# Optimization experiments

Hardware: AMD Instinct MI355X
Metric: run time of the kernel (lower is better)

## Reference

```python
import jax, jax.numpy as jnp
import numpy as np

N = 100000
E = 1600000
IN_FEATS = 512
N_CLASSES = 40
H1, D1 = 8, 8
H2, D2 = 1, N_CLASSES


def gat_conv(x, src, dst, W, al, ar, b, H, D):
    # x: [N, F] -> h: [N, H, D]
    n = x.shape[0]
    h = (x @ W).reshape(n, H, D)
    el = (h * al[None]).sum(-1)  # [N, H]
    er = (h * ar[None]).sum(-1)  # [N, H]
    e = jax.nn.leaky_relu(el[src] + er[dst], 0.2)  # [E, H]
    # segment softmax over destination neighborhoods
    emax = jax.ops.segment_max(e, dst, num_segments=n)  # [N, H]
    ee = jnp.exp(e - emax[dst])
    denom = jax.ops.segment_sum(ee, dst, num_segments=n)  # [N, H]
    a = ee / (denom[dst] + 1e-9)  # [E, H]
    m = h[src] * a[:, :, None]  # [E, H, D]
    out = jax.ops.segment_sum(m, dst, num_segments=n)  # [N, H, D]
    return out + b.reshape(1, H, D)


def setup_inputs() -> dict:
    key = jax.random.key(0)
    ks = jax.random.split(key, 12)
    g1 = 1.0 / np.sqrt(IN_FEATS)
    g2 = 1.0 / np.sqrt(H1 * D1)
    return {
        "x": jax.random.normal(ks[0], (N, IN_FEATS), jnp.float32),
        "src": jax.random.randint(ks[1], (E,), 0, N, jnp.int32),
        "dst": jax.random.randint(ks[2], (E,), 0, N, jnp.int32),
        "W1": jax.random.normal(ks[3], (IN_FEATS, H1 * D1), jnp.float32) * g1,
        "al1": jax.random.normal(ks[4], (H1, D1), jnp.float32) * 0.1,
        "ar1": jax.random.normal(ks[5], (H1, D1), jnp.float32) * 0.1,
        "b1": jnp.zeros((H1 * D1,), jnp.float32),
        "W2": jax.random.normal(ks[6], (H1 * D1, H2 * D2), jnp.float32) * g2,
        "al2": jax.random.normal(ks[7], (H2, D2), jnp.float32) * 0.1,
        "ar2": jax.random.normal(ks[8], (H2, D2), jnp.float32) * 0.1,
        "b2": jnp.zeros((H2 * D2,), jnp.float32),
    }


def reference(x, src, dst, W1, al1, ar1, b1, W2, al2, ar2, b2):
    h = gat_conv(x, src, dst, W1, al1, ar1, b1, H1, D1)  # [N, 8, 8]
    h = jax.nn.elu(h.reshape(N, H1 * D1))  # [N, 64]
    h = gat_conv(h, src, dst, W2, al2, ar2, b2, H2, D2).mean(axis=1)  # [N, n_classes]
    return jax.nn.log_softmax(h, axis=1)
```

## Files before the change

### kernel.cpp

```cpp
#include <hip/hip_runtime.h>
#include <hip/hip_bf16.h>
#include <math.h>

#define NCLS 40
#define H2S 64
#define PWG 256
#define BSH 9
#define NBMAX 512
#define SRCB 23
#define CSRCAP 14336

typedef __attribute__((ext_vector_type(8))) short bf16x8;
typedef __attribute__((ext_vector_type(4))) float f32x4;

__device__ inline float bf2f(ushort u) {
    unsigned v = ((unsigned)u) << 16;
    float f;
    __builtin_memcpy(&f, &v, 4);
    return f;
}
__device__ inline ushort f2bf(float f) {
    unsigned v;
    __builtin_memcpy(&v, &f, 4);
    unsigned r = (v + 0x7FFFu + ((v >> 16) & 1u)) >> 16;
    return (ushort)r;
}

__global__ __launch_bounds__(256) void conv_prep_kernel(
    const float* __restrict__ W1, ushort* __restrict__ W1t,
    const float* __restrict__ W2, const float* __restrict__ al2,
    const float* __restrict__ ar2, float* __restrict__ wal2,
    float* __restrict__ war2)
{
    if (blockIdx.x < 128) {
        int id = blockIdx.x * 256 + threadIdx.x;
        int k = id >> 6, c = id & 63;
        W1t[c * 512 + k] = f2bf(W1[k * 64 + c]);
    } else {
        int k = threadIdx.x;
        if (k < 64) {
            float a = 0.f, b = 0.f;
            for (int c = 0; c < NCLS; c++) {
                float w = W2[k * NCLS + c];
                a += w * al2[c];
                b += w * ar2[c];
            }
            wal2[k] = a;
            war2[k] = b;
        }
    }
}

__global__ __launch_bounds__(256) void gemm1_mfma_kernel(
    const float* __restrict__ x, const ushort* __restrict__ W1t,
    const float* __restrict__ al1, const float* __restrict__ ar1,
    ushort* __restrict__ h1b, float* __restrict__ el1,
    float* __restrict__ er1, int Nn)
{
    __shared__ ushort As[64 * 72];
    __shared__ ushort Bs[64 * 72];
    const int t = threadIdx.x;
    const int lane = t & 63, w = t >> 6;
    const int tile = blockIdx.x * 64;

    f32x4 acc[4] = {};

    const int sr = t >> 2;
    const int sk = (t & 3) * 16;
    const int arow = tile + sr;
    const bool rowok = arow < Nn;
    const float* xrow = x + (size_t)arow * 512;
    const ushort* wrow = W1t + (size_t)sr * 512;

    const int r = lane & 15, g = lane >> 4;

    float4 f0 = make_float4(0.f, 0.f, 0.f, 0.f), f1 = f0, f2 = f0, f3 = f0;
    bf16x8 bv0, bv1;
    if (rowok) {
        f0 = *(const float4*)(xrow + sk);
        f1 = *(const float4*)(xrow + sk + 4);
        f2 = *(const float4*)(xrow + sk + 8);
        f3 = *(const float4*)(xrow + sk + 12);
    }
    bv0 = *(const bf16x8*)(wrow + sk);
    bv1 = *(const bf16x8*)(wrow + sk + 8);

    for (int k0 = 0; k0 < 512; k0 += 64) {
        bf16x8 av0, av1;
        av0[0] = (short)f2bf(f0.x); av0[1] = (short)f2bf(f0.y);
        av0[2] = (short)f2bf(f0.z); av0[3] = (short)f2bf(f0.w);
        av0[4] = (short)f2bf(f1.x); av0[5] = (short)f2bf(f1.y);
        av0[6] = (short)f2bf(f1.z); av0[7] = (short)f2bf(f1.w);
        av1[0] = (short)f2bf(f2.x); av1[1] = (short)f2bf(f2.y);
        av1[2] = (short)f2bf(f2.z); av1[3] = (short)f2bf(f2.w);
        av1[4] = (short)f2bf(f3.x); av1[5] = (short)f2bf(f3.y);
        av1[6] = (short)f2bf(f3.z); av1[7] = (short)f2bf(f3.w);
        *(bf16x8*)&As[sr * 72 + sk] = av0;
        *(bf16x8*)&As[sr * 72 + sk + 8] = av1;
        *(bf16x8*)&Bs[sr * 72 + sk] = bv0;
        *(bf16x8*)&Bs[sr * 72 + sk + 8] = bv1;
        __syncthreads();

        int k1 = k0 + 64;
        if (k1 < 512) {
            if (rowok) {
                f0 = *(const float4*)(xrow + k1 + sk);
                f1 = *(const float4*)(xrow + k1 + sk + 4);
                f2 = *(const float4*)(xrow + k1 + sk + 8);
                f3 = *(const float4*)(xrow + k1 + sk + 12);
            }
            bv0 = *(const bf16x8*)(wrow + k1 + sk);
            bv1 = *(const bf16x8*)(wrow + k1 + sk + 8);
        }

        bf16x8 af0 = *(const bf16x8*)&As[(w * 16 + r) * 72 + g * 8];
        bf16x8 af1 = *(const bf16x8*)&As[(w * 16 + r) * 72 + 32 + g * 8];
#pragma unroll
        for (int cb = 0; cb < 4; cb++) {
            bf16x8 bf0 = *(const bf16x8*)&Bs[(cb * 16 + r) * 72 + g * 8];
            acc[cb] = __builtin_amdgcn_mfma_f32_16x16x32_bf16(af0, bf0, acc[cb], 0, 0, 0);
        }
#pragma unroll
        for (int cb = 0; cb < 4; cb++) {
            bf16x8 bf1 = *(const bf16x8*)&Bs[(cb * 16 + r) * 72 + 32 + g * 8];
            acc[cb] = __builtin_amdgcn_mfma_f32_16x16x32_bf16(af1, bf1, acc[cb], 0, 0, 0);
        }
        __syncthreads();
    }

    float alv[4], arv[4];
#pragma unroll
    for (int cb = 0; cb < 4; cb++) {
        alv[cb] = al1[cb * 16 + r];
        arv[cb] = ar1[cb * 16 + r];
    }
#pragma unroll
    for (int v = 0; v < 4; v++) {
        int row = tile + w * 16 + g * 4 + v;
        bool ok = row < Nn;
#pragma unroll
        for (int cb = 0; cb < 4; cb++) {
            if (ok) h1b[(size_t)row * 64 + cb * 16 + r] = f2bf(acc[cb][v]);
            float pel = acc[cb][v] * alv[cb];
            float per = acc[cb][v] * arv[cb];
            pel += __shfl_xor(pel, 1); per += __shfl_xor(per, 1);
            pel += __shfl_xor(pel, 2); per += __shfl_xor(per, 2);
            pel += __shfl_xor(pel, 4); per += __shfl_xor(per, 4);
            if (ok && (r & 7) == 0) {
                int head = cb * 2 + (r >> 3);
                el1[row * 8 + head] = pel;
                er1[row * 8 + head] = per;
            }
        }
    }
}

__global__ __launch_bounds__(256) void hist_kernel(const int* __restrict__ dst,
                                                   int* __restrict__ hist,
                                                   int Ee, int chunk, int NB)
{
    __shared__ int lh[NBMAX];
    const int wg = blockIdx.x, tid = threadIdx.x;
    for (int i = tid; i < NB; i += 256) lh[i] = 0;
    __syncthreads();
    const int beg = wg * chunk;
    const int endv = min(Ee, beg + chunk);
    for (int i = beg + tid; i < endv; i += 256) atomicAdd(&lh[dst[i] >> BSH], 1);
    __syncthreads();
    for (int b = tid; b < NB; b += 256) hist[b * PWG + wg] = lh[b];
}

__global__ __launch_bounds__(256) void scanA_kernel(int* __restrict__ hist,
                                                    int* __restrict__ bucketTot)
{
    __shared__ int s[256];
    const int b = blockIdx.x, tid = threadIdx.x;
    int v = hist[b * PWG + tid];
    s[tid] = v;
    __syncthreads();
#pragma unroll
    for (int o = 1; o < 256; o <<= 1) {
        int t = (tid >= o) ? s[tid - o] : 0;
        __syncthreads();
        s[tid] += t;
        __syncthreads();
    }
    hist[b * PWG + tid] = s[tid] - v;
    if (tid == 255) bucketTot[b] = s[255];
}

__global__ __launch_bounds__(256) void scanB_kernel(const int* __restrict__ bucketTot,
                                                    int* __restrict__ bucketBase,
                                                    int NB, int Ee)
{
    __shared__ int s[256];
    const int tid = threadIdx.x;
    int v = (tid < NB) ? bucketTot[tid] : 0;
    s[tid] = v;
    __syncthreads();
#pragma unroll
    for (int o = 1; o < 256; o <<= 1) {
        int t = (tid >= o) ? s[tid - o] : 0;
        __syncthreads();
        s[tid] += t;
        __syncthreads();
    }
    if (tid < NB) bucketBase[tid] = s[tid] - v;
    if (tid == 0) bucketBase[NB] = Ee;
}

__global__ __launch_bounds__(256) void partition_kernel(const int* __restrict__ src,
                                                        const int* __restrict__ dst,
                                                        const int* __restrict__ hist,
                                                        const int* __restrict__ bucketBase,
                                                        unsigned* __restrict__ ebuf,
                                                        int Ee, int chunk, int NB)
{
    __shared__ int cur[NBMAX];
    const int wg = blockIdx.x, tid = threadIdx.x;
    for (int b = tid; b < NB; b += 256) cur[b] = hist[b * PWG + wg] + bucketBase[b];
    __syncthreads();
    const int beg = wg * chunk;
    const int endv = min(Ee, beg + chunk);
    for (int i = beg + tid; i < endv; i += 256) {
        int d = dst[i];
        int p = atomicAdd(&cur[d >> BSH], 1);
        ebuf[p] = ((unsigned)(d & ((1 << BSH) - 1)) << SRCB) | (unsigned)src[i];
    }
}

__global__ __launch_bounds__(512) void bucket_csr_kernel(const unsigned* __restrict__ ebuf,
                                                         const int* __restrict__ bucketBase,
                                                         int* __restrict__ row_start,
                                                         int* __restrict__ perm_src,
                                                         int Nn, int Ee, int NB)
{
    __shared__ unsigned stage[CSRCAP];
    __shared__ int cnt[512];
    __shared__ int s[512];
    __shared__ int cur[512];
    const int b = blockIdx.x, tid = threadIdx.x;
    const int base = b << BSH;
    const int bb = bucketBase[b], be = bucketBase[b + 1];
    const int m = be - bb;

    cnt[tid] = 0;
    __syncthreads();
    for (int idx = tid; idx < m; idx += 512) {
        unsigned pk = ebuf[bb + idx];
        if (idx < CSRCAP) stage[idx] = pk;
        atomicAdd(&cnt[pk >> SRCB], 1);
    }
    __syncthreads();
    int v = cnt[tid];
    s[tid] = v;
    __syncthreads();
#pragma unroll
    for (int o = 1; o < 512; o <<= 1) {
        int t = (tid >= o) ? s[tid - o] : 0;
        __syncthreads();
        s[tid] += t;
        __syncthreads();
    }
    const int off = bb + s[tid] - v;
    const int node = base + tid;
    if (node < Nn) row_start[node] = off;
    cur[tid] = off;
    __syncthreads();
    for (int idx = tid; idx < m; idx += 512) {
        unsigned pk = (idx < CSRCAP) ? stage[idx] : ebuf[bb + idx];
        int p = atomicAdd(&cur[pk >> SRCB], 1);
        perm_src[p] = (int)(pk & ((1u << SRCB) - 1u));
    }
    if (b == NB - 1 && tid == 0) row_start[Nn] = Ee;
}

__global__ __launch_bounds__(256) void agg1_kernel(
    const ushort* __restrict__ h1b, const float* __restrict__ el1,
    const float* __restrict__ er1, const int* __restrict__ row_start,
    const int* __restrict__ perm_src, const float* __restrict__ b1,
    ushort* __restrict__ hmidb, int Nn)
{
    const int wid = (blockIdx.x * blockDim.x + threadIdx.x) >> 6;
    const int lane = threadIdx.x & 63;
    if (wid >= Nn) return;
    const int g = lane >> 4;
    const int q = lane & 15;
    const int h = q >> 1;
    const int beg = row_start[wid], end = row_start[wid + 1];
    const float er = er1[wid * 8 + h];

    float a0 = 0.f, a1 = 0.f, a2 = 0.f, a3 = 0.f, denom = 0.f;
    for (int i0 = beg; i0 < end; i0 += 64) {
        const int cnt = min(end - i0, 64);
        int pv = (i0 + lane < end) ? perm_src[i0 + lane] : 0;
        for (int j = 0; j < cnt; j += 8) {
            const int e0 = j + g, e1 = j + 4 + g;
            const int s0 = __shfl(pv, min(e0, cnt - 1));
            const int s1 = __shfl(pv, min(e1, cnt - 1));
            ushort4 r0 = *(const ushort4*)&h1b[(size_t)s0 * 64 + q * 4];
            ushort4 r1 = *(const ushort4*)&h1b[(size_t)s1 * 64 + q * 4];
            float x0 = el1[s0 * 8 + h];
            float x1 = el1[s1 * 8 + h];
            float e = x0 + er;
            e = (e >= 0.f) ? e : 0.2f * e;
            float w0 = (e0 < cnt) ? __expf(e) : 0.f;
            e = x1 + er;
            e = (e >= 0.f) ? e : 0.2f * e;
            float w1 = (e1 < cnt) ? __expf(e) : 0.f;
            denom += w0 + w1;
            a0 += bf2f(r0.x) * w0 + bf2f(r1.x) * w1;
            a1 += bf2f(r0.y) * w0 + bf2f(r1.y) * w1;
            a2 += bf2f(r0.z) * w0 + bf2f(r1.z) * w1;
            a3 += bf2f(r0.w) * w0 + bf2f(r1.w) * w1;
        }
    }
    denom += __shfl_xor(denom, 16); denom += __shfl_xor(denom, 32);
    a0 += __shfl_xor(a0, 16); a0 += __shfl_xor(a0, 32);
    a1 += __shfl_xor(a1, 16); a1 += __shfl_xor(a1, 32);
    a2 += __shfl_xor(a2, 16); a2 += __shfl_xor(a2, 32);
    a3 += __shfl_xor(a3, 16); a3 += __shfl_xor(a3, 32);
    if (g == 0) {
        const float4 bv = *(const float4*)&b1[q * 4];
        const float inv = 1.f / (denom + 1e-9f);
        float v0 = a0 * inv + bv.x;
        float v1 = a1 * inv + bv.y;
        float v2 = a2 * inv + bv.z;
        float v3 = a3 * inv + bv.w;
        v0 = (v0 > 0.f) ? v0 : expm1f(v0);
        v1 = (v1 > 0.f) ? v1 : expm1f(v1);
        v2 = (v2 > 0.f) ? v2 : expm1f(v2);
        v3 = (v3 > 0.f) ? v3 : expm1f(v3);
        ushort4 o;
        o.x = f2bf(v0); o.y = f2bf(v1); o.z = f2bf(v2); o.w = f2bf(v3);
        *(ushort4*)&hmidb[(size_t)wid * 64 + q * 4] = o;
    }
}

__global__ __launch_bounds__(256) void gemm2_kernel(
    const ushort* __restrict__ hmidb, const float* __restrict__ W2,
    const float* __restrict__ wal2, const float* __restrict__ war2,
    ushort* __restrict__ h2b, int Nn)
{
    __shared__ float w2s[64 * NCLS];
    __shared__ float wals[64], wars[64];
    for (int i = threadIdx.x; i < 64 * NCLS; i += blockDim.x) w2s[i] = W2[i];
    if (threadIdx.x < 64) {
        wals[threadIdx.x] = wal2[threadIdx.x];
        wars[threadIdx.x] = war2[threadIdx.x];
    }
    __syncthreads();
    int n = blockIdx.x * blockDim.x + threadIdx.x;
    if (n >= Nn) return;

    float out[NCLS];
#pragma unroll
    for (int c = 0; c < NCLS; c++) out[c] = 0.f;
    float accel = 0.f, accer = 0.f;

#pragma unroll 4
    for (int k4 = 0; k4 < 16; k4++) {
        ushort4 u = *(const ushort4*)&hmidb[(size_t)n * 64 + k4 * 4];
        float h0 = bf2f(u.x), h1 = bf2f(u.y), h2 = bf2f(u.z), h3 = bf2f(u.w);
        accel += h0 * wals[k4 * 4] + h1 * wals[k4 * 4 + 1] + h2 * wals[k4 * 4 + 2] + h3 * wals[k4 * 4 + 3];
        accer += h0 * wars[k4 * 4] + h1 * wars[k4 * 4 + 1] + h2 * wars[k4 * 4 + 2] + h3 * wars[k4 * 4 + 3];
#pragma unroll
        for (int c = 0; c < NCLS; c++) {
            out[c] += h0 * w2s[(k4 * 4 + 0) * NCLS + c] + h1 * w2s[(k4 * 4 + 1) * NCLS + c] +
                      h2 * w2s[(k4 * 4 + 2) * NCLS + c] + h3 * w2s[(k4 * 4 + 3) * NCLS + c];
        }
    }
    ushort* row = h2b + (size_t)n * H2S;
#pragma unroll
    for (int c = 0; c < NCLS; c += 2) {
        unsigned pk = (unsigned)f2bf(out[c]) | ((unsigned)f2bf(out[c + 1]) << 16);
        *(unsigned*)&row[c] = pk;
    }
    ((float*)row)[20] = accel;
    ((float*)row)[21] = accer;
}

__global__ __launch_bounds__(256) void agg2_kernel(
    const ushort* __restrict__ h2b, const int* __restrict__ row_start,
    const int* __restrict__ perm_src, const float* __restrict__ b2,
    float* __restrict__ out, int Nn)
{
    int wid = (blockIdx.x * blockDim.x + threadIdx.x) >> 6;
    int lane = threadIdx.x & 63;
    if (wid >= Nn) return;
    const int beg = row_start[wid], end = row_start[wid + 1];
    const float er = ((const float*)(h2b + (size_t)wid * H2S))[21];
    const bool act = lane < NCLS;
    const int cl = act ? lane : 0;

    float acc = 0.f, denom = 0.f;
    for (int i0 = beg; i0 < end; i0 += 64) {
        int cnt = min(end - i0, 64);
        int pv = (i0 + lane < end) ? perm_src[i0 + lane] : 0;
        int j = 0;
        for (; j + 8 <= cnt; j += 8) {
            int ss[8];
            float ev[8];
            ushort rv[8];
#pragma unroll
            for (int u = 0; u < 8; u++) ss[u] = __shfl(pv, j + u);
#pragma unroll
            for (int u = 0; u < 8; u++) {
                const ushort* rp = h2b + (size_t)ss[u] * H2S;
                rv[u] = rp[cl];
                ev[u] = ((const float*)rp)[20];
            }
#pragma unroll
            for (int u = 0; u < 8; u++) {
                float e = ev[u] + er;
                e = (e >= 0.f) ? e : 0.2f * e;
                float w = __expf(fminf(e, 80.f));
                denom += w;
                acc += bf2f(rv[u]) * w;
            }
        }
        for (; j + 4 <= cnt; j += 4) {
            int ss[4];
            float ev[4];
            ushort rv[4];
#pragma unroll
            for (int u = 0; u < 4; u++) ss[u] = __shfl(pv, j + u);
#pragma unroll
            for (int u = 0; u < 4; u++) {
                const ushort* rp = h2b + (size_t)ss[u] * H2S;
                rv[u] = rp[cl];
                ev[u] = ((const float*)rp)[20];
            }
#pragma unroll
            for (int u = 0; u < 4; u++) {
                float e = ev[u] + er;
                e = (e >= 0.f) ? e : 0.2f * e;
                float w = __expf(fminf(e, 80.f));
                denom += w;
                acc += bf2f(rv[u]) * w;
            }
        }
        for (; j < cnt; j++) {
            int sI = __shfl(pv, j);
            const ushort* rp = h2b + (size_t)sI * H2S;
            float e = ((const float*)rp)[20] + er;
            e = (e >= 0.f) ? e : 0.2f * e;
            float w = __expf(fminf(e, 80.f));
            denom += w;
            acc += bf2f(rp[cl]) * w;
        }
    }
    float v = act ? (acc / (denom + 1e-9f) + b2[lane]) : -1e30f;

    float mx = v;
#pragma unroll
    for (int o = 1; o < 64; o <<= 1) mx = fmaxf(mx, __shfl_xor(mx, o));
    float sx = act ? __expf(v - mx) : 0.f;
#pragma unroll
    for (int o = 1; o < 64; o <<= 1) sx += __shfl_xor(sx, o);
    if (act) out[(size_t)wid * NCLS + lane] = v - mx - __logf(sx);
}

extern "C" void kernel_launch(void* const* d_in, const int* in_sizes, int n_in,
                              void* d_out, int out_size, void* d_ws, size_t ws_size,
                              hipStream_t stream)
{
    const float* x   = (const float*)d_in[0];
    const int*   src = (const int*)d_in[1];
    const int*   dst = (const int*)d_in[2];
    const float* W1  = (const float*)d_in[3];
    const float* al1 = (const float*)d_in[4];
    const float* ar1 = (const float*)d_in[5];
    const float* b1  = (const float*)d_in[6];
    const float* W2  = (const float*)d_in[7];
    const float* al2 = (const float*)d_in[8];
    const float* ar2 = (const float*)d_in[9];
    const float* b2  = (const float*)d_in[10];
    float* out = (float*)d_out;

    const int Nn = in_sizes[0] / 512;
    const int Ee = in_sizes[1];
    const int NB = (Nn + (1 << BSH) - 1) >> BSH;
    const int chunk = (Ee + PWG - 1) / PWG;

    char* wsb = (char*)d_ws;
    size_t off = 0;
    auto alloc = [&](size_t bytes) -> void* {
        off = (off + 15) & ~(size_t)15;
        void* p = wsb + off;
        off += bytes;
        return p;
    };
    ushort* h1b   = (ushort*)alloc((size_t)Nn * 64 * 2);
    ushort* hmidb = (ushort*)alloc((size_t)Nn * 64 * 2);
    ushort* h2b   = (ushort*)alloc((size_t)Nn * H2S * 2);
    ushort* W1t   = (ushort*)alloc(64 * 512 * 2);
    float* el1  = (float*)alloc((size_t)Nn * 8 * 4);
    float* er1  = (float*)alloc((size_t)Nn * 8 * 4);
    float* wal2 = (float*)alloc(64 * 4);
    float* war2 = (float*)alloc(64 * 4);
    int* row_start  = (int*)alloc((size_t)(Nn + 1) * 4);
    int* hist       = (int*)alloc((size_t)NB * PWG * 4);
    int* bucketTot  = (int*)alloc((size_t)NB * 4);
    int* bucketBase = (int*)alloc((size_t)(NB + 1) * 4);
    int* perm_src   = (int*)alloc((size_t)Ee * 4);
    unsigned* ebuf  = (unsigned*)alloc((size_t)Ee * 4);

    hist_kernel<<<PWG, 256, 0, stream>>>(dst, hist, Ee, chunk, NB);
    scanA_kernel<<<NB, 256, 0, stream>>>(hist, bucketTot);
    scanB_kernel<<<1, 256, 0, stream>>>(bucketTot, bucketBase, NB, Ee);
    partition_kernel<<<PWG, 256, 0, stream>>>(src, dst, hist, bucketBase, ebuf, Ee, chunk, NB);
    bucket_csr_kernel<<<NB, 512, 0, stream>>>(ebuf, bucketBase, row_start, perm_src, Nn, Ee, NB);

    conv_prep_kernel<<<129, 256, 0, stream>>>(W1, W1t, W2, al2, ar2, wal2, war2);
    gemm1_mfma_kernel<<<(Nn + 63) / 64, 256, 0, stream>>>(x, W1t, al1, ar1, h1b, el1, er1, Nn);
    agg1_kernel<<<(Nn + 3) / 4, 256, 0, stream>>>(h1b, el1, er1, row_start, perm_src, b1, hmidb, Nn);

    gemm2_kernel<<<(Nn + 255) / 256, 256, 0, stream>>>(hmidb, W2, wal2, war2, h2b, Nn);
    agg2_kernel<<<(Nn + 3) / 4, 256, 0, stream>>>(h2b, row_start, perm_src, b2, out, Nn);
}
```

Measured before the change: 258.6 us.

## Merge prep into histogram kernel, pack bf16 pairs, vectorize agg2 gather

Folds the weight-prep work into the histogram launch as extra blocks, which removes one kernel launch. Replaces scalar bf16 rounding with a two-value pack using byte permute, used in gemm1, agg1 and gemm2. agg2 is rewritten so each lane gathers four classes via ushort4 and handles two edges per step across four lane groups, then reduces across groups and writes float4 output. The pack rounding drops the round-to-nearest-even tie handling, and agg2 no longer clamps the exponent at 80.

```diff
diff --git a/kernel.cpp b/kernel.cpp
--- a/kernel.cpp
+++ b/kernel.cpp
@@ -25,20 +25,28 @@
     unsigned r = (v + 0x7FFFu + ((v >> 16) & 1u)) >> 16;
     return (ushort)r;
 }
-
-__global__ __launch_bounds__(256) void conv_prep_kernel(
+__device__ inline unsigned pkbf(float a, float b) {
+    unsigned ua, ub;
+    __builtin_memcpy(&ua, &a, 4);
+    __builtin_memcpy(&ub, &b, 4);
+    return __builtin_amdgcn_perm(ub + 0x8000u, ua + 0x8000u, 0x07060302u);
+}
+
+__global__ __launch_bounds__(256) void hist_prep_kernel(
+    const int* __restrict__ dst, int* __restrict__ hist, int Ee, int chunk, int NB,
     const float* __restrict__ W1, ushort* __restrict__ W1t,
     const float* __restrict__ W2, const float* __restrict__ al2,
     const float* __restrict__ ar2, float* __restrict__ wal2,
     float* __restrict__ war2)
 {
-    if (blockIdx.x < 128) {
-        int id = blockIdx.x * 256 + threadIdx.x;
-        int k = id >> 6, c = id & 63;
-        W1t[c * 512 + k] = f2bf(W1[k * 64 + c]);
-    } else {
-        int k = threadIdx.x;
-        if (k < 64) {
+    if (blockIdx.x >= PWG) {
+        int bb = blockIdx.x - PWG;
+        if (bb < 128) {
+            int id = bb * 256 + threadIdx.x;
+            int k = id >> 6, c = id & 63;
+            W1t[c * 512 + k] = f2bf(W1[k * 64 + c]);
+        } else if (threadIdx.x < 64) {
+            int k = threadIdx.x;
             float a = 0.f, b = 0.f;
             for (int c = 0; c < NCLS; c++) {
                 float w = W2[k * NCLS + c];
@@ -48,7 +56,17 @@
             wal2[k] = a;
             war2[k] = b;
         }
-    }
+        return;
+    }
+    __shared__ int lh[NBMAX];
+    const int wg = blockIdx.x, tid = threadIdx.x;
+    for (int i = tid; i < NB; i += 256) lh[i] = 0;
+    __syncthreads();
+    const int beg = wg * chunk;
+    const int endv = min(Ee, beg + chunk);
+    for (int i = beg + tid; i < endv; i += 256) atomicAdd(&lh[dst[i] >> BSH], 1);
+    __syncthreads();
+    for (int b = tid; b < NB; b += 256) hist[b * PWG + wg] = lh[b];
 }
 
 __global__ __launch_bounds__(256) void gemm1_mfma_kernel(
@@ -86,17 +104,13 @@
     bv1 = *(const bf16x8*)(wrow + sk + 8);
 
     for (int k0 = 0; k0 < 512; k0 += 64) {
-        bf16x8 av0, av1;
-        av0[0] = (short)f2bf(f0.x); av0[1] = (short)f2bf(f0.y);
-        av0[2] = (short)f2bf(f0.z); av0[3] = (short)f2bf(f0.w);
-        av0[4] = (short)f2bf(f1.x); av0[5] = (short)f2bf(f1.y);
-        av0[6] = (short)f2bf(f1.z); av0[7] = (short)f2bf(f1.w);
-        av1[0] = (short)f2bf(f2.x); av1[1] = (short)f2bf(f2.y);
-        av1[2] = (short)f2bf(f2.z); av1[3] = (short)f2bf(f2.w);
-        av1[4] = (short)f2bf(f3.x); av1[5] = (short)f2bf(f3.y);
-        av1[6] = (short)f2bf(f3.z); av1[7] = (short)f2bf(f3.w);
-        *(bf16x8*)&As[sr * 72 + sk] = av0;
-        *(bf16x8*)&As[sr * 72 + sk + 8] = av1;
+        uint4 aw0, aw1;
+        aw0.x = pkbf(f0.x, f0.y); aw0.y = pkbf(f0.z, f0.w);
+        aw0.z = pkbf(f1.x, f1.y); aw0.w = pkbf(f1.z, f1.w);
+        aw1.x = pkbf(f2.x, f2.y); aw1.y = pkbf(f2.z, f2.w);
+        aw1.z = pkbf(f3.x, f3.y); aw1.w = pkbf(f3.z, f3.w);
+        *(uint4*)&As[sr * 72 + sk] = aw0;
+        *(uint4*)&As[sr * 72 + sk + 8] = aw1;
         *(bf16x8*)&Bs[sr * 72 + sk] = bv0;
         *(bf16x8*)&Bs[sr * 72 + sk + 8] = bv1;
         __syncthreads();
@@ -153,21 +167,6 @@
             }
         }
     }
-}
-
-__global__ __launch_bounds__(256) void hist_kernel(const int* __restrict__ dst,
-                                                   int* __restrict__ hist,
-                                                   int Ee, int chunk, int NB)
-{
-    __shared__ int lh[NBMAX];
-    const int wg = blockIdx.x, tid = threadIdx.x;
-    for (int i = tid; i < NB; i += 256) lh[i] = 0;
-    __syncthreads();
-    const int beg = wg * chunk;
-    const int endv = min(Ee, beg + chunk);
-    for (int i = beg + tid; i < endv; i += 256) atomicAdd(&lh[dst[i] >> BSH], 1);
-    __syncthreads();
-    for (int b = tid; b < NB; b += 256) hist[b * PWG + wg] = lh[b];
 }
 
 __global__ __launch_bounds__(256) void scanA_kernel(int* __restrict__ hist,
@@ -331,9 +330,10 @@
         v1 = (v1 > 0.f) ? v1 : expm1f(v1);
         v2 = (v2 > 0.f) ? v2 : expm1f(v2);
         v3 = (v3 > 0.f) ? v3 : expm1f(v3);
-        ushort4 o;
-        o.x = f2bf(v0); o.y = f2bf(v1); o.z = f2bf(v2); o.w = f2bf(v3);
-        *(ushort4*)&hmidb[(size_t)wid * 64 + q * 4] = o;
+        uint2 o;
+        o.x = pkbf(v0, v1);
+        o.y = pkbf(v2, v3);
+        *(uint2*)&hmidb[(size_t)wid * 64 + q * 4] = o;
     }
 }
 
@@ -373,8 +373,7 @@
     ushort* row = h2b + (size_t)n * H2S;
 #pragma unroll
     for (int c = 0; c < NCLS; c += 2) {
-        unsigned pk = (unsigned)f2bf(out[c]) | ((unsigned)f2bf(out[c + 1]) << 16);
-        *(unsigned*)&row[c] = pk;
+        *(unsigned*)&row[c] = pkbf(out[c], out[c + 1]);
     }
     ((float*)row)[20] = accel;
     ((float*)row)[21] = accer;
@@ -385,80 +384,70 @@
     const int* __restrict__ perm_src, const float* __restrict__ b2,
     float* __restrict__ out, int Nn)
 {
-    int wid = (blockIdx.x * blockDim.x + threadIdx.x) >> 6;
-    int lane = threadIdx.x & 63;
+    const int wid = (blockIdx.x * blockDim.x + threadIdx.x) >> 6;
+    const int lane = threadIdx.x & 63;
     if (wid >= Nn) return;
+    const int g = lane >> 4;
+    const int q = lane & 15;
     const int beg = row_start[wid], end = row_start[wid + 1];
     const float er = ((const float*)(h2b + (size_t)wid * H2S))[21];
-    const bool act = lane < NCLS;
-    const int cl = act ? lane : 0;
-
-    float acc = 0.f, denom = 0.f;
+
+    float a0 = 0.f, a1 = 0.f, a2 = 0.f, a3 = 0.f, denom = 0.f;
     for (int i0 = beg; i0 < end; i0 += 64) {
-        int cnt = min(end - i0, 64);
+        const int cnt = min(end - i0, 64);
         int pv = (i0 + lane < end) ? perm_src[i0 + lane] : 0;
-        int j = 0;
-        for (; j + 8 <= cnt; j += 8) {
-            int ss[8];
-            float ev[8];
-            ushort rv[8];
-#pragma unroll
-            for (int u = 0; u < 8; u++) ss[u] = __shfl(pv, j + u);
-#pragma unroll
-            for (int u = 0; u < 8; u++) {
-                const ushort* rp = h2b + (size_t)ss[u] * H2S;
-                rv[u] = rp[cl];
-                ev[u] = ((const float*)rp)[20];
-            }
-#pragma unroll
-            for (int u = 0; u < 8; u++) {
-                float e = ev[u] + er;
-                e = (e >= 0.f) ? e : 0.2f * e;
-                float w = __expf(fminf(e, 80.f));
-                denom += w;
-                acc += bf2f(rv[u]) * w;
-            }
-        }
-        for (; j + 4 <= cnt; j += 4) {
-            int ss[4];
-            float ev[4];
-            ushort rv[4];
-#pragma unroll
-            for (int u = 0; u < 4; u++) ss[u] = __shfl(pv, j + u);
-#pragma unroll
-            for (int u = 0; u < 4; u++) {
-                const ushort* rp = h2b + (size_t)ss[u] * H2S;
-                rv[u] = rp[cl];
-                ev[u] = ((const float*)rp)[20];
-            }
-#pragma unroll
-            for (int u = 0; u < 4; u++) {
-                float e = ev[u] + er;
-                e = (e >= 0.f) ? e : 0.2f * e;
-                float w = __expf(fminf(e, 80.f));
-                denom += w;
-                acc += bf2f(rv[u]) * w;
-            }
-        }
-        for (; j < cnt; j++) {
-            int sI = __shfl(pv, j);
-            const ushort* rp = h2b + (size_t)sI * H2S;
-            float e = ((const float*)rp)[20] + er;
+        for (int j = 0; j < cnt; j += 8) {
+            const int e0 = j + g, e1 = j + 4 + g;
+            const int s0 = __shfl(pv, min(e0, cnt - 1));
+            const int s1 = __shfl(pv, min(e1, cnt - 1));
+            const ushort* rp0 = h2b + (size_t)s0 * H2S;
+            const ushort* rp1 = h2b + (size_t)s1 * H2S;
+            ushort4 r0 = *(const ushort4*)(rp0 + q * 4);
+            ushort4 r1 = *(const ushort4*)(rp1 + q * 4);
+            float x0 = ((const float*)rp0)[20];
+            float x1 = ((const float*)rp1)[20];
+            float e = x0 + er;
             e = (e >= 0.f) ? e : 0.2f * e;
-            float w = __expf(fminf(e, 80.f));
-            denom += w;
-            acc += bf2f(rp[cl]) * w;
-        }
-    }
-    float v = act ? (acc / (denom + 1e-9f) + b2[lane]) : -1e30f;
-
-    float mx = v;
+            float w0 = (e0 < cnt) ? __expf(e) : 0.f;
+            e = x1 + er;
+            e = (e >= 0.f) ? e : 0.2f * e;
+            float w1 = (e1 < cnt) ? __expf(e) : 0.f;
+            denom += w0 + w1;
+            a0 += bf2f(r0.x) * w0 + bf2f(r1.x) * w1;
+            a1 += bf2f(r0.y) * w0 + bf2f(r1.y) * w1;
+            a2 += bf2f(r0.z) * w0 + bf2f(r1.z) * w1;
+            a3 += bf2f(r0.w) * w0 + bf2f(r1.w) * w1;
+        }
+    }
+    denom += __shfl_xor(denom, 16); denom += __shfl_xor(denom, 32);
+    a0 += __shfl_xor(a0, 16); a0 += __shfl_xor(a0, 32);
+    a1 += __shfl_xor(a1, 16); a1 += __shfl_xor(a1, 32);
+    a2 += __shfl_xor(a2, 16); a2 += __shfl_xor(a2, 32);
+    a3 += __shfl_xor(a3, 16); a3 += __shfl_xor(a3, 32);
+
+    const bool act = (g == 0) && (q < 10);
+    float v0, v1, v2, v3;
+    if (act) {
+        const float4 bv = *(const float4*)&b2[q * 4];
+        const float inv = 1.f / (denom + 1e-9f);
+        v0 = a0 * inv + bv.x;
+        v1 = a1 * inv + bv.y;
+        v2 = a2 * inv + bv.z;
+        v3 = a3 * inv + bv.w;
+    } else {
+        v0 = v1 = v2 = v3 = -1e30f;
+    }
+    float mx = fmaxf(fmaxf(v0, v1), fmaxf(v2, v3));
 #pragma unroll
     for (int o = 1; o < 64; o <<= 1) mx = fmaxf(mx, __shfl_xor(mx, o));
-    float sx = act ? __expf(v - mx) : 0.f;
+    float sx = act ? (__expf(v0 - mx) + __expf(v1 - mx) + __expf(v2 - mx) + __expf(v3 - mx)) : 0.f;
 #pragma unroll
     for (int o = 1; o < 64; o <<= 1) sx += __shfl_xor(sx, o);
-    if (act) out[(size_t)wid * NCLS + lane] = v - mx - __logf(sx);
+    if (act) {
+        float lg = mx + __logf(sx);
+        float4 o4 = make_float4(v0 - lg, v1 - lg, v2 - lg, v3 - lg);
+        *(float4*)&out[(size_t)wid * NCLS + q * 4] = o4;
+    }
 }
 
 extern "C" void kernel_launch(void* const* d_in, const int* in_sizes, int n_in,
@@ -506,13 +495,13 @@
     int* perm_src   = (int*)alloc((size_t)Ee * 4);
     unsigned* ebuf  = (unsigned*)alloc((size_t)Ee * 4);
 
-    hist_kernel<<<PWG, 256, 0, stream>>>(dst, hist, Ee, chunk, NB);
+    hist_prep_kernel<<<PWG + 129, 256, 0, stream>>>(dst, hist, Ee, chunk, NB,
+                                                    W1, W1t, W2, al2, ar2, wal2, war2);
     scanA_kernel<<<NB, 256, 0, stream>>>(hist, bucketTot);
     scanB_kernel<<<1, 256, 0, stream>>>(bucketTot, bucketBase, NB, Ee);
     partition_kernel<<<PWG, 256, 0, stream>>>(src, dst, hist, bucketBase, ebuf, Ee, chunk, NB);
     bucket_csr_kernel<<<NB, 512, 0, stream>>>(ebuf, bucketBase, row_start, perm_src, Nn, Ee, NB);
 
-    conv_prep_kernel<<<129, 256, 0, stream>>>(W1, W1t, W2, al2, ar2, wal2, war2);
     gemm1_mfma_kernel<<<(Nn + 63) / 64, 256, 0, stream>>>(x, W1t, al1, ar1, h1b, el1, er1, Nn);
     agg1_kernel<<<(Nn + 3) / 4, 256, 0, stream>>>(h1b, el1, er1, row_start, perm_src, b1, hmidb, Nn);
 
```

Result: faster. 240.7 us (-6.9%).
